# Optimization experiments

Measured on AMD Instinct MI355X. Metric: run time of the kernel, lower is better.

Reference implementation:

```python
import jax, jax.numpy as jnp
import numpy as np

E = 256      # embed size
H = 256      # hidden size
V_SRC = 32000
V_TGT = 32000
B = 32
S_SRC = 512
S_TGT = 128
PAD = 0


def lstm_cell(x, h, c, Wih, Whh, b):
    # PyTorch gate order: i, f, g, o
    g = x @ Wih.T + h @ Whh.T + b
    i, f, gg, o = jnp.split(g, 4, axis=-1)
    c = jax.nn.sigmoid(f) * c + jax.nn.sigmoid(i) * jnp.tanh(gg)
    h = jax.nn.sigmoid(o) * jnp.tanh(c)
    return h, c


def run_lstm(X, Wih, Whh, b):
    # X: (S, B, E) -> outs (S, B, H), final (h, c)
    Bq = X.shape[1]
    h0 = jnp.zeros((Bq, H), X.dtype)
    c0 = jnp.zeros((Bq, H), X.dtype)

    def step(carry, xt):
        h, c = carry
        h, c = lstm_cell(xt, h, c, Wih, Whh, b)
        return (h, c), h

    (hF, cF), outs = jax.lax.scan(step, (h0, c0), X)
    return outs, hF, cF


def setup_inputs() -> dict:
    key = jax.random.key(0)
    ks = jax.random.split(key, 20)
    s = 0.05
    inp = {
        "source": jax.random.randint(ks[0], (S_SRC, B), 0, V_SRC, dtype=jnp.int32),
        "target": jax.random.randint(ks[1], (S_TGT, B), 0, V_TGT, dtype=jnp.int32),
        "src_emb": jax.random.normal(ks[2], (V_SRC, E)) * s,
        "tgt_emb": jax.random.normal(ks[3], (V_TGT, E)) * s,
        "Wih_f": jax.random.normal(ks[4], (4 * H, E)) * s,
        "Whh_f": jax.random.normal(ks[5], (4 * H, H)) * s,
        "b_f": jax.random.normal(ks[6], (4 * H,)) * s,
        "Wih_b": jax.random.normal(ks[7], (4 * H, E)) * s,
        "Whh_b": jax.random.normal(ks[8], (4 * H, H)) * s,
        "b_b": jax.random.normal(ks[9], (4 * H,)) * s,
        "Wih_d": jax.random.normal(ks[10], (4 * H, E + H)) * s,
        "Whh_d": jax.random.normal(ks[11], (4 * H, H)) * s,
        "b_d": jax.random.normal(ks[12], (4 * H,)) * s,
        "Wh": jax.random.normal(ks[13], (H, 2 * H)) * s,
        "Wc": jax.random.normal(ks[14], (H, 2 * H)) * s,
        "Watt": jax.random.normal(ks[15], (H, 2 * H)) * s,
        "Wcomb": jax.random.normal(ks[16], (H, 3 * H)) * s,
        "Wvoc": jax.random.normal(ks[17], (V_TGT, H)) * s,
    }
    return inp


def reference(source, target, src_emb, tgt_emb, Wih_f, Whh_f, b_f,
              Wih_b, Whh_b, b_b, Wih_d, Whh_d, b_d,
              Wh, Wc, Watt, Wcomb, Wvoc):
    # ---- encode ----
    X = src_emb[source]                       # (S_src, B, E)
    outs_f, hF, _ = run_lstm(X, Wih_f, Whh_f, b_f)
    outs_b, hB, _ = run_lstm(X[::-1], Wih_b, Whh_b, b_b)
    outs_b = outs_b[::-1]
    enc_hiddens = jnp.concatenate([outs_f, outs_b], axis=-1)  # (S, B, 2H)
    enc_hiddens = jnp.transpose(enc_hiddens, (1, 0, 2))       # (B, S, 2H)
    h_t = jnp.concatenate([hF, hB], axis=-1) @ Wh.T           # (B, H)
    c_t = jnp.concatenate([hF, hB], axis=-1) @ Wc.T
    # all source lengths == S_SRC -> no positions masked
    enc_masks = jnp.zeros((enc_hiddens.shape[0], enc_hiddens.shape[1]), bool)
    enc_hiddens_proj = enc_hiddens @ Watt.T                   # (B, S, H)

    # ---- decode ----
    Y = tgt_emb[target[:-1]]                  # (T, B, E), T = S_TGT-1
    o0 = jnp.zeros((enc_hiddens.shape[0], H), X.dtype)

    def step(carry, y_t):
        h, c, o_prev = carry
        i_t = jnp.concatenate([y_t, o_prev], axis=-1)
        h, c = lstm_cell(i_t, h, c, Wih_d, Whh_d, b_d)
        e_t = jnp.einsum('bsh,bh->bs', enc_hiddens_proj, h)
        e_t = jnp.where(enc_masks, -jnp.inf, e_t)
        a_t = jax.nn.softmax(e_t, axis=-1)
        ctx = jnp.einsum('bs,bsd->bd', a_t, enc_hiddens)       # (B, 2H)
        o_t = jnp.tanh(jnp.concatenate([h, ctx], axis=-1) @ Wcomb.T)
        # dropout is identity (rate 0 / eval)
        return (h, c, o_t), o_t

    _, hidden_outs = jax.lax.scan(step, (h_t, c_t, o0), Y)    # (T, B, H)

    logits = hidden_outs @ Wvoc.T                              # (T, B, V)
    P = jax.nn.log_softmax(logits, axis=-1)
    idx = target[1:]                                           # (T, B)
    lp = jnp.take_along_axis(P, idx[..., None], axis=-1)[..., 0]
    tgt_mask = (idx != PAD).astype(P.dtype)
    scores = (lp * tgt_mask).sum(axis=0)                       # (B,)
    return scores
```

## Files before the change

kernel.cpp:

```cpp
#include <hip/hip_runtime.h>
#include <hip/hip_bf16.h>
#include <math.h>

typedef unsigned int u32;
typedef unsigned short u16;
typedef __attribute__((ext_vector_type(8))) short bf16x8;
typedef __attribute__((ext_vector_type(4))) float f32x4;

__device__ __forceinline__ float bfbits(u32 hi) { union { u32 u; float f; } v; v.u = hi; return v.f; }
__device__ __forceinline__ float lo16(u32 p) { return bfbits(p << 16); }
__device__ __forceinline__ float hi16(u32 p) { return bfbits(p & 0xffff0000u); }
__device__ __forceinline__ float b2f(u16 x) { return bfbits(((u32)x) << 16); }
__device__ __forceinline__ u16 f2b(float f) {
    union { float f; u32 u; } v; v.f = f;
    u32 u = v.u;
    u32 r = (u + 0x7fffu + ((u >> 16) & 1u)) >> 16;
    return (u16)r;
}
__device__ __forceinline__ float cvtf(float x) { return x; }
__device__ __forceinline__ float cvtf(u16 x) { return b2f(x); }
__device__ __forceinline__ void storef(float* p, float v) { *p = v; }
__device__ __forceinline__ void storef(u16* p, float v) { *p = f2b(v); }
__device__ __forceinline__ float sigf(float x) { return 1.f / (1.f + expf(-x)); }
__device__ __forceinline__ float dotq(uint4 q, const float* p) {
    float4 a = *(const float4*)p;
    float4 b = *(const float4*)(p + 4);
    return lo16(q.x) * a.x + hi16(q.x) * a.y + lo16(q.y) * a.z + hi16(q.y) * a.w
         + lo16(q.z) * b.x + hi16(q.z) * b.y + lo16(q.w) * b.z + hi16(q.w) * b.w;
}
__device__ __forceinline__ float red8(float a) {
    a += __shfl_xor(a, 1);
    a += __shfl_xor(a, 2);
    a += __shfl_xor(a, 4);
    return a;
}
__device__ __forceinline__ void ast(float* p, float v) {
    __hip_atomic_store(p, v, __ATOMIC_RELAXED, __HIP_MEMORY_SCOPE_AGENT);
}
__device__ __forceinline__ float ald(const float* p) {
    return __hip_atomic_load((float*)p, __ATOMIC_RELAXED, __HIP_MEMORY_SCOPE_AGENT);
}

__global__ void k_detect(const void* __restrict__ emb, int* __restrict__ flag) {
    __shared__ int s;
    if (threadIdx.x == 0) s = 0;
    __syncthreads();
    const u16* p = (const u16*)emb;
    int bad = 0;
    for (int i = threadIdx.x; i < 8192; i += 256) {
        float v = b2f(p[i]);
        if (!(fabsf(v) < 1e4f)) bad = 1;
    }
    if (bad) s = 1;
    __syncthreads();
    if (threadIdx.x == 0) *flag = s;
}

__global__ void k_conv(const void* __restrict__ src, u16* __restrict__ dst, int n,
                       const int* __restrict__ flag) {
    int i = blockIdx.x * 256 + threadIdx.x;
    if (i >= n) return;
    if (*flag) dst[i] = f2b(((const float*)src)[i]);
    else       dst[i] = ((const u16*)src)[i];
}

__global__ void k_wattT(const void* __restrict__ src, u16* __restrict__ dst,
                        const int* __restrict__ flag) {
    int c = blockIdx.x;
    int r = threadIdx.x;
    u16 v;
    if (*flag) v = f2b(((const float*)src)[(size_t)r * 512 + c]);
    else       v = ((const u16*)src)[(size_t)r * 512 + c];
    dst[(size_t)c * 256 + r] = v;
}

__global__ void k_embed(const int* __restrict__ tok, const void* __restrict__ emb,
                        u16* __restrict__ out, const int* __restrict__ flag) {
    int row = blockIdx.x;
    int e = threadIdx.x;
    int v = tok[row];
    u16 r;
    if (*flag) r = f2b(((const float*)emb)[(size_t)v * 256 + e]);
    else       r = ((const u16*)emb)[(size_t)v * 256 + e];
    out[(size_t)row * 256 + e] = r;
}

template <typename TA, typename TC>
__global__ __launch_bounds__(256) void k_gemm_nt(
    const TA* __restrict__ A, int lda,
    const u16* __restrict__ B, int ldb,
    const u16* __restrict__ bias,
    TC* __restrict__ C, int ldc,
    int M, int N, int K) {
    __shared__ float As[32][68];
    __shared__ float Bs[32][68];
    const int bm = blockIdx.y * 64, bn = blockIdx.x * 64;
    const int tid = threadIdx.x;
    const int tm = (tid & 15) * 4, tn = (tid >> 4) * 4;
    float acc[4][4] = {};
    const int ml = tid >> 2, kl = (tid & 3) * 8;
    for (int k0 = 0; k0 < K; k0 += 32) {
        {
            float v[8];
            if (bm + ml < M) {
                const TA* ap = A + (size_t)(bm + ml) * lda + (k0 + kl);
#pragma unroll
                for (int i = 0; i < 8; i++) v[i] = cvtf(ap[i]);
            } else {
#pragma unroll
                for (int i = 0; i < 8; i++) v[i] = 0.f;
            }
#pragma unroll
            for (int i = 0; i < 8; i++) As[kl + i][ml] = v[i];
        }
        {
            float v[8];
            if (bn + ml < N) {
                const u16* bp = B + (size_t)(bn + ml) * ldb + (k0 + kl);
#pragma unroll
                for (int i = 0; i < 8; i++) v[i] = b2f(bp[i]);
            } else {
#pragma unroll
                for (int i = 0; i < 8; i++) v[i] = 0.f;
            }
#pragma unroll
            for (int i = 0; i < 8; i++) Bs[kl + i][ml] = v[i];
        }
        __syncthreads();
#pragma unroll
        for (int k = 0; k < 32; k++) {
            float4 av = *(const float4*)&As[k][tm];
            float4 bv = *(const float4*)&Bs[k][tn];
            acc[0][0] += av.x * bv.x; acc[0][1] += av.x * bv.y; acc[0][2] += av.x * bv.z; acc[0][3] += av.x * bv.w;
            acc[1][0] += av.y * bv.x; acc[1][1] += av.y * bv.y; acc[1][2] += av.y * bv.z; acc[1][3] += av.y * bv.w;
            acc[2][0] += av.z * bv.x; acc[2][1] += av.z * bv.y; acc[2][2] += av.z * bv.z; acc[2][3] += av.z * bv.w;
            acc[3][0] += av.w * bv.x; acc[3][1] += av.w * bv.y; acc[3][2] += av.w * bv.z; acc[3][3] += av.w * bv.w;
        }
        __syncthreads();
    }
#pragma unroll
    for (int i = 0; i < 4; i++) {
        int m = bm + tm + i;
        if (m >= M) continue;
#pragma unroll
        for (int j = 0; j < 4; j++) {
            int n = bn + tn + j;
            float v = acc[i][j];
            if (bias) v += b2f(bias[n]);
            storef(&C[(size_t)m * ldc + n], v);
        }
    }
}

__device__ __forceinline__ void gbar(int* c, int target) {
    __syncthreads();
    if (threadIdx.x == 0) {
        __hip_atomic_fetch_add(c, 1, __ATOMIC_RELAXED, __HIP_MEMORY_SCOPE_AGENT);
        while (__hip_atomic_load(c, __ATOMIC_RELAXED, __HIP_MEMORY_SCOPE_AGENT) < target)
            __builtin_amdgcn_s_sleep(2);
    }
    __syncthreads();
}

__global__ __launch_bounds__(512) void k_enc_mb(
    const u16* __restrict__ Xf, const u16* __restrict__ Xb,
    const u16* __restrict__ Whh_f, const u16* __restrict__ Whh_b,
    u16* __restrict__ enc, float* __restrict__ hFB,
    float* __restrict__ gbe, int* __restrict__ cnte) {
    const int chain = blockIdx.x & 63, gi = blockIdx.x >> 6;
    const int d = chain >> 5, b = chain & 31;
    const int j = threadIdx.x;
    const int q = j & 7, r8i = j >> 3;
    __shared__ u16 whl[256 * 264];
    __shared__ float hs[256];
    __shared__ float gall4[4][64];
    const u16* W = d ? Whh_b : Whh_f;
    for (int idx = j; idx < 8192; idx += 512) {
        int row = idx >> 5, kc = idx & 31;
        int grow = (row >> 6) * 256 + gi * 64 + (row & 63);
        *(uint4*)&whl[row * 264 + kc * 8] =
            *(const uint4*)(W + (size_t)grow * 256 + kc * 8);
    }
    float c = 0.f;
    if (j < 256) hs[j] = 0.f;
    __syncthreads();
    const u16* Xd = d ? Xb : Xf;
    float* hb = gbe + (size_t)chain * 512;
    int* cc = cnte + chain * 32;
    for (int step = 0; step < 512; step++) {
        const int pos = d ? (511 - step) : step;
        const u16* xp = Xd + ((size_t)pos * 32 + b) * 1024;
#pragma unroll 2
        for (int it = 0; it < 4; it++) {
            const u16* wr = &whl[(it * 64 + r8i) * 264];
            float a0 = 0.f, a1 = 0.f;
#pragma unroll
            for (int i = 0; i < 4; i += 2) {
                int u0 = q + 8 * i, u1 = q + 8 * (i + 1);
                a0 += dotq(*(const uint4*)(wr + u0 * 8), &hs[u0 * 8]);
                a1 += dotq(*(const uint4*)(wr + u1 * 8), &hs[u1 * 8]);
            }
            float a = red8(a0 + a1);
            if (q == 0) gall4[it][r8i] = a + b2f(xp[it * 256 + gi * 64 + r8i]);
        }
        __syncthreads();
        if (j < 64) {
            int jj = gi * 64 + j;
            float ig = sigf(gall4[0][j]), fg = sigf(gall4[1][j]);
            float gg = tanhf(gall4[2][j]), og = sigf(gall4[3][j]);
            c = fg * c + ig * gg;
            float h = og * tanhf(c);
            ast(&hb[(step & 1) * 256 + jj], h);
            enc[((size_t)b * 512 + pos) * 512 + (size_t)d * 256 + jj] = f2b(h);
        }
        gbar(cc, 4 * (step + 1));
        if (j < 256) hs[j] = ald(&hb[(step & 1) * 256 + j]);
        __syncthreads();
    }
    if (gi == 0 && j < 256) hFB[(size_t)b * 512 + (size_t)d * 256 + j] = hs[j];
}

__global__ __launch_bounds__(512) void k_dec_mb(
    const u16* __restrict__ Ypart,
    const u16* __restrict__ Whh_d, const u16* __restrict__ Wih_d,
    const u16* __restrict__ WattT, const u16* __restrict__ Wcomb,
    const u16* __restrict__ enc,
    const float* __restrict__ ht0, const float* __restrict__ ct0,
    float* __restrict__ hid,
    float* __restrict__ hbd, float* __restrict__ evsum,
    float* __restrict__ pctx, int* __restrict__ cnt) {
    const int b = blockIdx.x & 31, gi = blockIdx.x >> 5;
    const int j = threadIdx.x;
    const int q = j & 7, r8i = j >> 3;
    const int wv = j >> 6, ln = j & 63;
    __shared__ u16 encl[128 * 520];
    __shared__ float hs[256], os[256];
    __shared__ float g[512];
    __shared__ float evl[128];
    __shared__ float pctxw[8][520];
    __shared__ float hc[768];
    __shared__ float redw[8];
    __shared__ float gall4[4][64];
    float c = 0.f;
    if (j < 256) {
        hs[j] = ht0[(size_t)b * 256 + j];
        os[j] = 0.f;
    }
    if (j < 64) c = ct0[(size_t)b * 256 + gi * 64 + j];
    {
        const uint4* encb = (const uint4*)(enc + (size_t)b * 512 * 512);
        for (int idx = j; idx < 8192; idx += 512) {
            int row = idx >> 6, kc = idx & 63;
            *(uint4*)&encl[row * 520 + kc * 8] = encb[(size_t)(gi * 128 + row) * 64 + kc];
        }
    }
    __syncthreads();
    float* hb = hbd + (size_t)b * 512;
    int* c0 = cnt + b * 32;
    for (int s = 0; s < 127; s++) {
        const int tgt = 4 * (s + 1);
        const u16* yp = Ypart + ((size_t)s * 32 + b) * 1024;
#pragma unroll 2
        for (int it = 0; it < 4; it++) {
            int row = it * 256 + gi * 64 + r8i;
            const uint4* wh = (const uint4*)(Whh_d + (size_t)row * 256);
            const uint4* wo = (const uint4*)(Wih_d + (size_t)row * 512 + 256);
            float ah = 0.f, ao = 0.f;
#pragma unroll
            for (int i = 0; i < 4; i++) {
                int u = q + 8 * i;
                ah += dotq(wh[u], &hs[u * 8]);
                ao += dotq(wo[u], &os[u * 8]);
            }
            float a = red8(ah + ao);
            if (q == 0) gall4[it][r8i] = a + b2f(yp[row]);
        }
        __syncthreads();
        if (j < 64) {
            int jj = gi * 64 + j;
            float ig = sigf(gall4[0][j]), fg = sigf(gall4[1][j]);
            float gg = tanhf(gall4[2][j]), og = sigf(gall4[3][j]);
            c = fg * c + ig * gg;
            float h = og * tanhf(c);
            ast(&hb[(s & 1) * 256 + jj], h);
        }
        gbar(c0, tgt);
        if (j < 256) hs[j] = ald(&hb[(s & 1) * 256 + j]);
        __syncthreads();
#pragma unroll 4
        for (int it = 0; it < 8; it++) {
            int row = it * 64 + r8i;
            const uint4* wt = (const uint4*)(WattT + (size_t)row * 256);
            float a0 = 0.f, a1 = 0.f;
#pragma unroll
            for (int i = 0; i < 4; i += 2) {
                int u0 = q + 8 * i, u1 = q + 8 * (i + 1);
                a0 += dotq(wt[u0], &hs[u0 * 8]);
                a1 += dotq(wt[u1], &hs[u1 * 8]);
            }
            float a = red8(a0 + a1);
            if (q == 0) g[row] = a;
        }
        __syncthreads();
#pragma unroll 2
        for (int it = 0; it < 2; it++) {
            int lrow = it * 64 + r8i;
            const u16* er = &encl[lrow * 520];
            float a0 = 0.f, a1 = 0.f;
#pragma unroll
            for (int i = 0; i < 8; i += 2) {
                int u0 = q + 8 * i, u1 = q + 8 * (i + 1);
                a0 += dotq(*(const uint4*)(er + u0 * 8), &g[u0 * 8]);
                a1 += dotq(*(const uint4*)(er + u1 * 8), &g[u1 * 8]);
            }
            float a = red8(a0 + a1);
            if (q == 0) evl[lrow] = expf(a);
        }
        __syncthreads();
        if (j < 64) {
            float v = evl[j] + evl[j + 64];
            for (int off = 32; off; off >>= 1) v += __shfl_down(v, off);
            if (j == 0) ast(&evsum[b * 16 + gi], v);
        }
        {
            float a0 = 0, a1 = 0, a2 = 0, a3 = 0, a4 = 0, a5 = 0, a6 = 0, a7 = 0;
#pragma unroll 4
            for (int rr = 0; rr < 16; rr++) {
                int lrow = wv * 16 + rr;
                uint4 qd = *(const uint4*)&encl[lrow * 520 + ln * 8];
                float w = evl[lrow];
                a0 += w * lo16(qd.x); a1 += w * hi16(qd.x);
                a2 += w * lo16(qd.y); a3 += w * hi16(qd.y);
                a4 += w * lo16(qd.z); a5 += w * hi16(qd.z);
                a6 += w * lo16(qd.w); a7 += w * hi16(qd.w);
            }
            float* pw = &pctxw[wv][ln * 8];
            pw[0] = a0; pw[1] = a1; pw[2] = a2; pw[3] = a3;
            pw[4] = a4; pw[5] = a5; pw[6] = a6; pw[7] = a7;
        }
        __syncthreads();
        if (j < 512) {
            float p = 0.f;
#pragma unroll
            for (int w = 0; w < 8; w++) p += pctxw[w][j];
            ast(&pctx[((size_t)b * 4 + gi) * 512 + j], p);
        }
        gbar(c0 + 16, tgt);
        if (j < 4) redw[j] = ald(&evsum[b * 16 + j]);
        if (j < 256) hc[j] = hs[j];
        __syncthreads();
        if (j < 512) {
            const float* pc = pctx + (size_t)b * 4 * 512;
            float v = ald(&pc[j]) + ald(&pc[512 + j]) + ald(&pc[1024 + j]) + ald(&pc[1536 + j]);
            hc[256 + j] = v / (redw[0] + redw[1] + redw[2] + redw[3]);
        }
        __syncthreads();
#pragma unroll 2
        for (int it = 0; it < 4; it++) {
            int row = it * 64 + r8i;
            const uint4* wc = (const uint4*)(Wcomb + (size_t)row * 768);
            float a0 = 0.f, a1 = 0.f;
#pragma unroll
            for (int i = 0; i < 12; i += 2) {
                int u0 = q + 8 * i, u1 = q + 8 * (i + 1);
                a0 += dotq(wc[u0], &hc[u0 * 8]);
                a1 += dotq(wc[u1], &hc[u1 * 8]);
            }
            float a = red8(a0 + a1);
            if (q == 0) {
                float o = tanhf(a);
                os[row] = o;
                if (gi == 0) hid[((size_t)s * 32 + b) * 256 + row] = o;
            }
        }
        __syncthreads();
    }
}

__global__ __launch_bounds__(256) void k_lidx(
    const int* __restrict__ target, const float* __restrict__ hid,
    const void* __restrict__ WvocV, float* __restrict__ lidx,
    const int* __restrict__ flag) {
    int p = blockIdx.x * 4 + (threadIdx.x >> 6);
    if (p >= 127 * 32) return;
    int lane = threadIdx.x & 63;
    int t = p >> 5, b = p & 31;
    int idx = target[(t + 1) * 32 + b];
    const float* h = hid + (size_t)p * 256;
    const bool f32w = (*flag != 0);
    float a = 0.f;
#pragma unroll
    for (int i = 0; i < 4; i++) {
        int k = lane * 4 + i;
        float wv = f32w ? ((const float*)WvocV)[(size_t)idx * 256 + k]
                        : b2f(((const u16*)WvocV)[(size_t)idx * 256 + k]);
        a += h[k] * wv;
    }
    for (int off = 32; off; off >>= 1) a += __shfl_down(a, off);
    if (lane == 0) lidx[p] = a;
}

__global__ __launch_bounds__(256) void k_sumexp(
    const float* __restrict__ hid, const void* __restrict__ WvocV,
    float* __restrict__ psum, const int* __restrict__ flag) {
    const int cb = blockIdx.x * 128;
    const int tid = threadIdx.x;
    const bool f32w = (*flag != 0);
    __shared__ u16 Wl[128 * 264];
    __shared__ u16 Hsb[32 * 264];
    __shared__ float red[32][2];
    for (int idx = tid; idx < 4096; idx += 256) {
        int col = idx >> 5, kc = idx & 31;
        uint4 val;
        if (f32w) {
            const float4* src = (const float4*)((const float*)WvocV + (size_t)(cb + col) * 256 + kc * 8);
            float4 f0 = src[0], f1 = src[1];
            u16 h[8];
            h[0] = f2b(f0.x); h[1] = f2b(f0.y); h[2] = f2b(f0.z); h[3] = f2b(f0.w);
            h[4] = f2b(f1.x); h[5] = f2b(f1.y); h[6] = f2b(f1.z); h[7] = f2b(f1.w);
            val = *(const uint4*)h;
        } else {
            val = *(const uint4*)((const u16*)WvocV + (size_t)(cb + col) * 256 + kc * 8);
        }
        *(uint4*)&Wl[col * 264 + kc * 8] = val;
    }
    const int wave = tid >> 6, lane = tid & 63;
    const int mtile = wave & 1;
    const int n0base = (wave >> 1) * 64;
    const int fr = lane & 15, fk = (lane >> 4) * 8;
    const int drow = mtile * 16 + (lane >> 4) * 4;
    for (int it = 0; it < 127; it++) {
        const int gr = it * 32;
        __syncthreads();
        for (int idx = tid; idx < 1024; idx += 256) {
            int row = idx >> 5, kq = idx & 31;
            const float4* hp = (const float4*)(hid + (size_t)(gr + row) * 256 + kq * 8);
            float4 f0 = hp[0], f1 = hp[1];
            u16 h[8];
            h[0] = f2b(f0.x); h[1] = f2b(f0.y); h[2] = f2b(f0.z); h[3] = f2b(f0.w);
            h[4] = f2b(f1.x); h[5] = f2b(f1.y); h[6] = f2b(f1.z); h[7] = f2b(f1.w);
            *(uint4*)&Hsb[row * 264 + kq * 8] = *(const uint4*)h;
        }
        __syncthreads();
        bf16x8 afr[8];
#pragma unroll
        for (int kc = 0; kc < 8; kc++)
            afr[kc] = *(const bf16x8*)&Hsb[(mtile * 16 + fr) * 264 + kc * 32 + fk];
        float es[4] = {0.f, 0.f, 0.f, 0.f};
#pragma unroll
        for (int nt = 0; nt < 4; nt++) {
            f32x4 acc = {0.f, 0.f, 0.f, 0.f};
            const u16* bbase = &Wl[(n0base + nt * 16 + fr) * 264 + fk];
#pragma unroll
            for (int kc = 0; kc < 8; kc++) {
                bf16x8 bfr = *(const bf16x8*)(bbase + kc * 32);
                acc = __builtin_amdgcn_mfma_f32_16x16x32_bf16(afr[kc], bfr, acc, 0, 0, 0);
            }
#pragma unroll
            for (int r = 0; r < 4; r++) es[r] += expf(acc[r]);
        }
#pragma unroll
        for (int r = 0; r < 4; r++) {
            float v = es[r];
            v += __shfl_xor(v, 1);
            v += __shfl_xor(v, 2);
            v += __shfl_xor(v, 4);
            v += __shfl_xor(v, 8);
            if ((lane & 15) == 0) red[drow + r][wave >> 1] = v;
        }
        __syncthreads();
        if (tid < 32) atomicAdd(&psum[gr + tid], red[tid][0] + red[tid][1]);
    }
}

__global__ void k_scores(const int* __restrict__ target, const float* __restrict__ lidx,
                         const float* __restrict__ psum, void* __restrict__ outv,
                         const int* __restrict__ flag) {
    int b = threadIdx.x;
    if (b >= 32) return;
    float acc = 0.f;
    for (int t = 0; t < 127; t++) {
        int idx = target[(t + 1) * 32 + b];
        if (idx != 0) {
            int row = t * 32 + b;
            acc += lidx[row] - logf(psum[row]);
        }
    }
    if (*flag) ((float*)outv)[b] = acc;
    else       ((u16*)outv)[b] = f2b(acc);
}

extern "C" void kernel_launch(void* const* d_in, const int* in_sizes, int n_in,
                              void* d_out, int out_size, void* d_ws, size_t ws_size,
                              hipStream_t stream) {
    const int* source = (const int*)d_in[0];
    const int* target = (const int*)d_in[1];
    const void* src_emb = d_in[2];
    const void* tgt_emb = d_in[3];
    const void* Wih_f = d_in[4];
    const void* Whh_f = d_in[5];
    const void* b_f = d_in[6];
    const void* Wih_b = d_in[7];
    const void* Whh_b = d_in[8];
    const void* b_b = d_in[9];
    const void* Wih_d = d_in[10];
    const void* Whh_d = d_in[11];
    const void* b_d = d_in[12];
    const void* Wh = d_in[13];
    const void* Wc = d_in[14];
    const void* Watt = d_in[15];
    const void* Wcomb = d_in[16];
    const void* Wvoc = d_in[17];

    int* flag = (int*)d_ws;
    float* fw = (float*)d_ws;
    size_t off = 64;
    float* hid = fw + off;    off += (size_t)127 * 32 * 256;
    float* hFB = fw + off;    off += (size_t)32 * 512;
    float* ht0 = fw + off;    off += (size_t)32 * 256;
    float* ct0 = fw + off;    off += (size_t)32 * 256;
    float* lidx = fw + off;   off += 4096;
    float* psum = fw + off;   off += 4096;
    float* hbd = fw + off;    off += (size_t)32 * 512;
    float* evsum = fw + off;  off += 512;
    float* pctx = fw + off;   off += (size_t)32 * 4 * 512;
    float* gbe = fw + off;    off += (size_t)64 * 512;
    int* cnt = (int*)(fw + off); off += 1024;
    int* cnte = (int*)(fw + off); off += 2048;
    u16* ub = (u16*)(fw + off);
    size_t uo = 0;
    u16* X = ub + uo;       uo += (size_t)512 * 32 * 256;
    u16* Yemb = ub + uo;    uo += (size_t)127 * 32 * 256;
    u16* Xf = ub + uo;      uo += (size_t)512 * 32 * 1024;
    u16* Xb = ub + uo;      uo += (size_t)512 * 32 * 1024;
    u16* Ypart = ub + uo;   uo += (size_t)127 * 32 * 1024;
    u16* enc_p = ub + uo;   uo += (size_t)32 * 512 * 512;
    u16* WattT = ub + uo;   uo += 131072;
    u16* cWih_f = ub + uo;  uo += 262144;
    u16* cWhh_f = ub + uo;  uo += 262144;
    u16* cb_f = ub + uo;    uo += 1024;
    u16* cWih_b = ub + uo;  uo += 262144;
    u16* cWhh_b = ub + uo;  uo += 262144;
    u16* cb_b = ub + uo;    uo += 1024;
    u16* cWih_d = ub + uo;  uo += 524288;
    u16* cWhh_d = ub + uo;  uo += 262144;
    u16* cb_d = ub + uo;    uo += 1024;
    u16* cWh = ub + uo;     uo += 131072;
    u16* cWc = ub + uo;     uo += 131072;
    u16* cWcomb = ub + uo;  uo += 196608;
    size_t needed = off * 4 + uo * 2;
    if (ws_size < needed) return;

    k_detect<<<1, 256, 0, stream>>>(src_emb, flag);
    auto conv = [&](const void* s, u16* d, int n) {
        k_conv<<<(n + 255) / 256, 256, 0, stream>>>(s, d, n, flag);
    };
    conv(Wih_f, cWih_f, 262144);  conv(Whh_f, cWhh_f, 262144);  conv(b_f, cb_f, 1024);
    conv(Wih_b, cWih_b, 262144);  conv(Whh_b, cWhh_b, 262144);  conv(b_b, cb_b, 1024);
    conv(Wih_d, cWih_d, 524288);  conv(Whh_d, cWhh_d, 262144);  conv(b_d, cb_d, 1024);
    conv(Wh, cWh, 131072);        conv(Wc, cWc, 131072);
    conv(Wcomb, cWcomb, 196608);
    k_wattT<<<512, 256, 0, stream>>>(Watt, WattT, flag);

    k_embed<<<512 * 32, 256, 0, stream>>>(source, src_emb, X, flag);
    k_gemm_nt<u16, u16><<<dim3(16, 256), 256, 0, stream>>>(X, 256, cWih_f, 256, cb_f, Xf, 1024, 16384, 1024, 256);
    k_gemm_nt<u16, u16><<<dim3(16, 256), 256, 0, stream>>>(X, 256, cWih_b, 256, cb_b, Xb, 1024, 16384, 1024, 256);
    hipMemsetAsync(cnte, 0, 2048 * sizeof(int), stream);
    k_enc_mb<<<256, 512, 0, stream>>>(Xf, Xb, cWhh_f, cWhh_b, enc_p, hFB, gbe, cnte);
    k_gemm_nt<float, float><<<dim3(4, 1), 256, 0, stream>>>(hFB, 512, cWh, 512, (const u16*)nullptr, ht0, 256, 32, 256, 512);
    k_gemm_nt<float, float><<<dim3(4, 1), 256, 0, stream>>>(hFB, 512, cWc, 512, (const u16*)nullptr, ct0, 256, 32, 256, 512);
    k_embed<<<127 * 32, 256, 0, stream>>>(target, tgt_emb, Yemb, flag);
    k_gemm_nt<u16, u16><<<dim3(16, 64), 256, 0, stream>>>(Yemb, 256, cWih_d, 512, cb_d, Ypart, 1024, 4064, 1024, 256);
    hipMemsetAsync(cnt, 0, 1024 * sizeof(int), stream);
    k_dec_mb<<<128, 512, 0, stream>>>(Ypart, cWhh_d, cWih_d, WattT, cWcomb, enc_p,
                                      ht0, ct0, hid, hbd, evsum, pctx, cnt);
    hipMemsetAsync(psum, 0, 4096 * sizeof(float), stream);
    k_lidx<<<(127 * 32 + 3) / 4, 256, 0, stream>>>(target, hid, Wvoc, lidx, flag);
    k_sumexp<<<250, 256, 0, stream>>>(hid, Wvoc, psum, flag);
    k_scores<<<1, 64, 0, stream>>>(target, lidx, psum, d_out, flag);
}
```

Measured before the change: 4.560 ms.

## Precompute attention projection of encoder states and split decoder across eight blocks

Adds a GEMM that computes enc_hiddens_proj = enc @ Watt^T once before decoding and stores it in a new buffer. The decoder then computes attention scores directly against cached projection rows in LDS, which replaces the per-step Watt^T·h matvec and the 512-wide score dot product. The decoder grid also grows from 4 to 8 blocks per batch item, each owning 32 hidden units and 64 source positions. This reduces per-step work and LDS use per block, but adds a global barrier participant per group and more cross-block partial-sum traffic.

```diff
diff --git a/kernel.cpp b/kernel.cpp
--- a/kernel.cpp
+++ b/kernel.cpp
@@ -62,16 +62,6 @@
     if (i >= n) return;
     if (*flag) dst[i] = f2b(((const float*)src)[i]);
     else       dst[i] = ((const u16*)src)[i];
-}
-
-__global__ void k_wattT(const void* __restrict__ src, u16* __restrict__ dst,
-                        const int* __restrict__ flag) {
-    int c = blockIdx.x;
-    int r = threadIdx.x;
-    u16 v;
-    if (*flag) v = f2b(((const float*)src)[(size_t)r * 512 + c]);
-    else       v = ((const u16*)src)[(size_t)r * 512 + c];
-    dst[(size_t)c * 256 + r] = v;
 }
 
 __global__ void k_embed(const int* __restrict__ tok, const void* __restrict__ emb,
@@ -223,7 +213,7 @@
 __global__ __launch_bounds__(512) void k_dec_mb(
     const u16* __restrict__ Ypart,
     const u16* __restrict__ Whh_d, const u16* __restrict__ Wih_d,
-    const u16* __restrict__ WattT, const u16* __restrict__ Wcomb,
+    const u16* __restrict__ projg, const u16* __restrict__ Wcomb,
     const u16* __restrict__ enc,
     const float* __restrict__ ht0, const float* __restrict__ ct0,
     float* __restrict__ hid,
@@ -233,36 +223,43 @@
     const int j = threadIdx.x;
     const int q = j & 7, r8i = j >> 3;
     const int wv = j >> 6, ln = j & 63;
-    __shared__ u16 encl[128 * 520];
+    __shared__ u16 encl[64 * 520];
+    __shared__ u16 projl[64 * 264];
     __shared__ float hs[256], os[256];
-    __shared__ float g[512];
-    __shared__ float evl[128];
+    __shared__ float evl[64];
     __shared__ float pctxw[8][520];
     __shared__ float hc[768];
     __shared__ float redw[8];
-    __shared__ float gall4[4][64];
+    __shared__ float gall[128];
     float c = 0.f;
     if (j < 256) {
         hs[j] = ht0[(size_t)b * 256 + j];
         os[j] = 0.f;
     }
-    if (j < 64) c = ct0[(size_t)b * 256 + gi * 64 + j];
+    if (j < 32) c = ct0[(size_t)b * 256 + gi * 32 + j];
     {
         const uint4* encb = (const uint4*)(enc + (size_t)b * 512 * 512);
-        for (int idx = j; idx < 8192; idx += 512) {
+        for (int idx = j; idx < 4096; idx += 512) {
             int row = idx >> 6, kc = idx & 63;
-            *(uint4*)&encl[row * 520 + kc * 8] = encb[(size_t)(gi * 128 + row) * 64 + kc];
+            *(uint4*)&encl[row * 520 + kc * 8] = encb[(size_t)(gi * 64 + row) * 64 + kc];
+        }
+        const uint4* projb = (const uint4*)(projg + (size_t)b * 512 * 256);
+        for (int idx = j; idx < 2048; idx += 512) {
+            int row = idx >> 5, kc = idx & 31;
+            *(uint4*)&projl[row * 264 + kc * 8] = projb[(size_t)(gi * 64 + row) * 32 + kc];
         }
     }
     __syncthreads();
     float* hb = hbd + (size_t)b * 512;
     int* c0 = cnt + b * 32;
     for (int s = 0; s < 127; s++) {
-        const int tgt = 4 * (s + 1);
+        const int tgt = 8 * (s + 1);
         const u16* yp = Ypart + ((size_t)s * 32 + b) * 1024;
-#pragma unroll 2
-        for (int it = 0; it < 4; it++) {
-            int row = it * 256 + gi * 64 + r8i;
+#pragma unroll
+        for (int it = 0; it < 2; it++) {
+            int rl = it * 64 + r8i;
+            int gate = rl >> 5, jj = gi * 32 + (rl & 31);
+            int row = gate * 256 + jj;
             const uint4* wh = (const uint4*)(Whh_d + (size_t)row * 256);
             const uint4* wo = (const uint4*)(Wih_d + (size_t)row * 512 + 256);
             float ah = 0.f, ao = 0.f;
@@ -273,13 +270,13 @@
                 ao += dotq(wo[u], &os[u * 8]);
             }
             float a = red8(ah + ao);
-            if (q == 0) gall4[it][r8i] = a + b2f(yp[row]);
-        }
-        __syncthreads();
-        if (j < 64) {
-            int jj = gi * 64 + j;
-            float ig = sigf(gall4[0][j]), fg = sigf(gall4[1][j]);
-            float gg = tanhf(gall4[2][j]), og = sigf(gall4[3][j]);
+            if (q == 0) gall[rl] = a + b2f(yp[row]);
+        }
+        __syncthreads();
+        if (j < 32) {
+            int jj = gi * 32 + j;
+            float ig = sigf(gall[j]), fg = sigf(gall[32 + j]);
+            float gg = tanhf(gall[64 + j]), og = sigf(gall[96 + j]);
             c = fg * c + ig * gg;
             float h = og * tanhf(c);
             ast(&hb[(s & 1) * 256 + jj], h);
@@ -287,46 +284,29 @@
         gbar(c0, tgt);
         if (j < 256) hs[j] = ald(&hb[(s & 1) * 256 + j]);
         __syncthreads();
-#pragma unroll 4
-        for (int it = 0; it < 8; it++) {
-            int row = it * 64 + r8i;
-            const uint4* wt = (const uint4*)(WattT + (size_t)row * 256);
+        {
+            const u16* pr = &projl[r8i * 264];
             float a0 = 0.f, a1 = 0.f;
 #pragma unroll
             for (int i = 0; i < 4; i += 2) {
                 int u0 = q + 8 * i, u1 = q + 8 * (i + 1);
-                a0 += dotq(wt[u0], &hs[u0 * 8]);
-                a1 += dotq(wt[u1], &hs[u1 * 8]);
+                a0 += dotq(*(const uint4*)(pr + u0 * 8), &hs[u0 * 8]);
+                a1 += dotq(*(const uint4*)(pr + u1 * 8), &hs[u1 * 8]);
             }
             float a = red8(a0 + a1);
-            if (q == 0) g[row] = a;
-        }
-        __syncthreads();
-#pragma unroll 2
-        for (int it = 0; it < 2; it++) {
-            int lrow = it * 64 + r8i;
-            const u16* er = &encl[lrow * 520];
-            float a0 = 0.f, a1 = 0.f;
-#pragma unroll
-            for (int i = 0; i < 8; i += 2) {
-                int u0 = q + 8 * i, u1 = q + 8 * (i + 1);
-                a0 += dotq(*(const uint4*)(er + u0 * 8), &g[u0 * 8]);
-                a1 += dotq(*(const uint4*)(er + u1 * 8), &g[u1 * 8]);
-            }
-            float a = red8(a0 + a1);
-            if (q == 0) evl[lrow] = expf(a);
+            if (q == 0) evl[r8i] = expf(a);
         }
         __syncthreads();
         if (j < 64) {
-            float v = evl[j] + evl[j + 64];
+            float v = evl[j];
             for (int off = 32; off; off >>= 1) v += __shfl_down(v, off);
             if (j == 0) ast(&evsum[b * 16 + gi], v);
         }
         {
             float a0 = 0, a1 = 0, a2 = 0, a3 = 0, a4 = 0, a5 = 0, a6 = 0, a7 = 0;
-#pragma unroll 4
-            for (int rr = 0; rr < 16; rr++) {
-                int lrow = wv * 16 + rr;
+#pragma unroll
+            for (int rr = 0; rr < 8; rr++) {
+                int lrow = wv * 8 + rr;
                 uint4 qd = *(const uint4*)&encl[lrow * 520 + ln * 8];
                 float w = evl[lrow];
                 a0 += w * lo16(qd.x); a1 += w * hi16(qd.x);
@@ -343,16 +323,20 @@
             float p = 0.f;
 #pragma unroll
             for (int w = 0; w < 8; w++) p += pctxw[w][j];
-            ast(&pctx[((size_t)b * 4 + gi) * 512 + j], p);
+            ast(&pctx[((size_t)b * 8 + gi) * 512 + j], p);
         }
         gbar(c0 + 16, tgt);
-        if (j < 4) redw[j] = ald(&evsum[b * 16 + j]);
+        if (j < 8) redw[j] = ald(&evsum[b * 16 + j]);
         if (j < 256) hc[j] = hs[j];
         __syncthreads();
-        if (j < 512) {
-            const float* pc = pctx + (size_t)b * 4 * 512;
-            float v = ald(&pc[j]) + ald(&pc[512 + j]) + ald(&pc[1024 + j]) + ald(&pc[1536 + j]);
-            hc[256 + j] = v / (redw[0] + redw[1] + redw[2] + redw[3]);
+        {
+            const float* pc = pctx + (size_t)b * 8 * 512;
+            float v = 0.f;
+#pragma unroll
+            for (int g2 = 0; g2 < 8; g2++) v += ald(&pc[g2 * 512 + j]);
+            float inv = 1.f / (redw[0] + redw[1] + redw[2] + redw[3] +
+                               redw[4] + redw[5] + redw[6] + redw[7]);
+            hc[256 + j] = v * inv;
         }
         __syncthreads();
 #pragma unroll 2
@@ -523,7 +507,7 @@
     float* psum = fw + off;   off += 4096;
     float* hbd = fw + off;    off += (size_t)32 * 512;
     float* evsum = fw + off;  off += 512;
-    float* pctx = fw + off;   off += (size_t)32 * 4 * 512;
+    float* pctx = fw + off;   off += (size_t)32 * 8 * 512;
     float* gbe = fw + off;    off += (size_t)64 * 512;
     int* cnt = (int*)(fw + off); off += 1024;
     int* cnte = (int*)(fw + off); off += 2048;
@@ -535,7 +519,8 @@
     u16* Xb = ub + uo;      uo += (size_t)512 * 32 * 1024;
     u16* Ypart = ub + uo;   uo += (size_t)127 * 32 * 1024;
     u16* enc_p = ub + uo;   uo += (size_t)32 * 512 * 512;
-    u16* WattT = ub + uo;   uo += 131072;
+    u16* proj = ub + uo;    uo += (size_t)32 * 512 * 256;
+    u16* cWatt = ub + uo;   uo += 131072;
     u16* cWih_f = ub + uo;  uo += 262144;
     u16* cWhh_f = ub + uo;  uo += 262144;
     u16* cb_f = ub + uo;    uo += 1024;
@@ -559,20 +544,20 @@
     conv(Wih_b, cWih_b, 262144);  conv(Whh_b, cWhh_b, 262144);  conv(b_b, cb_b, 1024);
     conv(Wih_d, cWih_d, 524288);  conv(Whh_d, cWhh_d, 262144);  conv(b_d, cb_d, 1024);
     conv(Wh, cWh, 131072);        conv(Wc, cWc, 131072);
-    conv(Wcomb, cWcomb, 196608);
-    k_wattT<<<512, 256, 0, stream>>>(Watt, WattT, flag);
+    conv(Watt, cWatt, 131072);    conv(Wcomb, cWcomb, 196608);
 
     k_embed<<<512 * 32, 256, 0, stream>>>(source, src_emb, X, flag);
     k_gemm_nt<u16, u16><<<dim3(16, 256), 256, 0, stream>>>(X, 256, cWih_f, 256, cb_f, Xf, 1024, 16384, 1024, 256);
     k_gemm_nt<u16, u16><<<dim3(16, 256), 256, 0, stream>>>(X, 256, cWih_b, 256, cb_b, Xb, 1024, 16384, 1024, 256);
     hipMemsetAsync(cnte, 0, 2048 * sizeof(int), stream);
     k_enc_mb<<<256, 512, 0, stream>>>(Xf, Xb, cWhh_f, cWhh_b, enc_p, hFB, gbe, cnte);
+    k_gemm_nt<u16, u16><<<dim3(4, 256), 256, 0, stream>>>(enc_p, 512, cWatt, 512, (const u16*)nullptr, proj, 256, 16384, 256, 512);
     k_gemm_nt<float, float><<<dim3(4, 1), 256, 0, stream>>>(hFB, 512, cWh, 512, (const u16*)nullptr, ht0, 256, 32, 256, 512);
     k_gemm_nt<float, float><<<dim3(4, 1), 256, 0, stream>>>(hFB, 512, cWc, 512, (const u16*)nullptr, ct0, 256, 32, 256, 512);
     k_embed<<<127 * 32, 256, 0, stream>>>(target, tgt_emb, Yemb, flag);
     k_gemm_nt<u16, u16><<<dim3(16, 64), 256, 0, stream>>>(Yemb, 256, cWih_d, 512, cb_d, Ypart, 1024, 4064, 1024, 256);
     hipMemsetAsync(cnt, 0, 1024 * sizeof(int), stream);
-    k_dec_mb<<<128, 512, 0, stream>>>(Ypart, cWhh_d, cWih_d, WattT, cWcomb, enc_p,
+    k_dec_mb<<<256, 512, 0, stream>>>(Ypart, cWhh_d, cWih_d, proj, cWcomb, enc_p,
                                       ht0, ct0, hid, hbd, evsum, pctx, cnt);
     hipMemsetAsync(psum, 0, 4096 * sizeof(float), stream);
     k_lidx<<<(127 * 32 + 3) / 4, 256, 0, stream>>>(target, hid, Wvoc, lidx, flag);
```

New measurement: 5.950 ms. 30.5% more time.
